# Kernel tuning notes

Measured on AMD Instinct MI355X. Metric: run time of the kernel, lower is better.

The kernel has to match this reference:

```python
import jax, jax.numpy as jnp
import numpy as np

N, E, D, H = 40000, 640000, 128, 8
DH = D // H  # out_feats per head
EPS = 1e-5


def _layernorm(x, g, b):
    mu = jnp.mean(x, axis=-1, keepdims=True)
    var = jnp.mean(jnp.square(x - mu), axis=-1, keepdims=True)
    return (x - mu) * jax.lax.rsqrt(var + EPS) * g + b


def setup_inputs() -> dict:
    key = jax.random.key(0)
    ks = jax.random.split(key, 12)
    s = 0.02
    return {
        "feat": jax.random.normal(ks[0], (N, D), dtype=jnp.float32),
        "src": jax.random.randint(ks[1], (E,), 0, N, dtype=jnp.int32),
        "dst": jax.random.randint(ks[2], (E,), 0, N, dtype=jnp.int32),
        "Wq": jax.random.normal(ks[3], (D, D), dtype=jnp.float32) * s,
        "Wk": jax.random.normal(ks[4], (D, D), dtype=jnp.float32) * s,
        "Wv": jax.random.normal(ks[5], (D, D), dtype=jnp.float32) * s,
        "ln1_g": jnp.ones((D,), jnp.float32),
        "ln1_b": jnp.zeros((D,), jnp.float32),
        "ln2_g": jnp.ones((D,), jnp.float32),
        "ln2_b": jnp.zeros((D,), jnp.float32),
        "W1": jax.random.normal(ks[6], (D, 4 * D), dtype=jnp.float32) * s,
        "b1": jnp.zeros((4 * D,), jnp.float32),
        "prelu_w": jnp.full((4 * D,), 0.25, jnp.float32),
        "W2": jax.random.normal(ks[7], (4 * D, D), dtype=jnp.float32) * s,
        "b2": jnp.zeros((D,), jnp.float32),
    }


def reference(feat, src, dst, Wq, Wk, Wv, ln1_g, ln1_b, ln2_g, ln2_b,
              W1, b1, prelu_w, W2, b2):
    n = feat.shape[0]
    feat_c = jax.lax.stop_gradient(feat)  # .clone().detach()
    q = (feat @ Wq).reshape(n, H, DH)
    k = (feat_c @ Wk).reshape(n, H, DH)
    v = (feat_c @ Wv).reshape(n, H, DH)

    # u_dot_v: per-edge, per-head dot product of k at src and q at dst
    scores = jnp.einsum('ehd,ehd->eh', k[src], q[dst]) / np.float32(np.sqrt(DH * H))

    # edge_softmax: softmax over incoming edges of each destination node
    smax = jax.ops.segment_max(scores, dst, num_segments=n)  # [N,H]
    sexp = jnp.exp(scores - smax[dst])
    ssum = jax.ops.segment_sum(sexp, dst, num_segments=n)
    a = sexp / ssum[dst]  # [E,H]  (attn_drop is eval no-op)

    # u_mul_e + sum: weighted scatter-aggregate of v[src] into dst
    msgs = v[src] * a[:, :, None]  # [E,H,DH]
    ft2 = jax.ops.segment_sum(msgs, dst, num_segments=n).reshape(n, D)

    rst = _layernorm(ft2 + feat, ln1_g, ln1_b)
    h = rst @ W1 + b1
    h = jnp.where(h >= 0, h, prelu_w * h)  # PReLU, per-channel
    ffn = h @ W2 + b2  # ffn_drop is eval no-op
    return _layernorm(rst + ffn, ln2_g, ln2_b)
```

## Files before the change

### kernel.cpp

```cpp
#include <hip/hip_runtime.h>
#include <hip/hip_bf16.h>
#include <math.h>

#define DIM 128
#define NHEAD 8
#define DHEAD 16
#define HID 512
#define LN_EPS 1e-5f
#define QSCALE 0.12751879104863297f

typedef __bf16 bf16x8 __attribute__((ext_vector_type(8)));
typedef float f32x4 __attribute__((ext_vector_type(4)));
typedef float f32x2 __attribute__((ext_vector_type(2)));
typedef _Float16 f16x2 __attribute__((ext_vector_type(2)));

__device__ inline float bf2f(unsigned int bits16) {
    return __uint_as_float(bits16 << 16);
}
__device__ inline unsigned short f2bf(float f) {
    unsigned int u = __float_as_uint(f);
    unsigned int r = u + 0x7fff + ((u >> 16) & 1);
    return (unsigned short)(r >> 16);
}
__device__ inline unsigned short f2h(float f) {
    _Float16 h = (_Float16)f;
    return __builtin_bit_cast(unsigned short, h);
}
__device__ inline unsigned short pk_fp8(float a, float b) {
    int r = __builtin_amdgcn_cvt_pk_fp8_f32(a, b, 0, false);
    return (unsigned short)(r & 0xffff);
}
template <bool HI>
__device__ inline f32x2 unpk_fp8(unsigned int w) {
    return __builtin_amdgcn_cvt_pk_f32_fp8((int)w, HI);
}
__device__ inline float fexp2(float x) { return __builtin_amdgcn_exp2f(x); }

__device__ inline void gload_lds16(const void* g, void* l) {
    __builtin_amdgcn_global_load_lds(
        (const __attribute__((address_space(1))) unsigned int*)g,
        (__attribute__((address_space(3))) unsigned int*)l, 16, 0, 0);
}

__global__ __launch_bounds__(256) void prep_kernel(
        int* counts, int Nn,
        const float* __restrict__ feat, unsigned short* __restrict__ featb,
        const float* __restrict__ Wq, const float* __restrict__ Wk, const float* __restrict__ Wv,
        unsigned short* __restrict__ Wqkvt,
        const float* __restrict__ W1, unsigned short* __restrict__ W1t,
        const float* __restrict__ W2, unsigned short* __restrict__ W2t,
        int zb, int fb) {
    int blk = blockIdx.x, t = threadIdx.x;
    if (blk < zb) {
        int i = blk * 1024 + t * 4;
        if (i < Nn) *(int4*)(counts + i) = make_int4(0, 0, 0, 0);
    } else if (blk < fb) {
        int i = (blk - zb) * 256 + t;
        if (i < Nn * 32) {
            float4 v = *(const float4*)(feat + (size_t)i * 4);
            ushort4 o;
            o.x = f2bf(v.x); o.y = f2bf(v.y); o.z = f2bf(v.z); o.w = f2bf(v.w);
            *(ushort4*)(featb + (size_t)i * 4) = o;
        }
    } else {
        int b2_ = blk - fb;
        if (b2_ < 192) {
            int sec = b2_ >> 6;
            const float* W = sec == 0 ? Wq : (sec == 1 ? Wk : Wv);
            int o = (b2_ & 63) * 256 + t;
            int oc = o >> 7, orow = o & 127;
            Wqkvt[sec * 16384 + o] = f2bf(W[(size_t)orow * 128 + oc]);
        } else if (b2_ < 448) {
            int o = (b2_ - 192) * 256 + t;
            int oc = o >> 7, orow = o & 127;
            W1t[o] = f2bf(W1[(size_t)orow * 512 + oc]);
        } else {
            int o = (b2_ - 448) * 256 + t;
            int oc = o >> 9, orow = o & 511;
            W2t[o] = f2bf(W2[(size_t)orow * 128 + oc]);
        }
    }
}


__global__ void count_kernel(const int* __restrict__ dst, int* counts, int E) {
    int e = blockIdx.x * blockDim.x + threadIdx.x;
    if (e < E) atomicAdd(&counts[dst[e]], 1);
}

__global__ __launch_bounds__(256) void scanA_kernel(const int* __restrict__ counts, int* bsum, int Nn) {
    int blk = blockIdx.x, t = threadIdx.x;
    int i = blk * 1024 + t * 4;
    int s = 0;
    if (i < Nn) { int4 x = *(const int4*)(counts + i); s = x.x + x.y + x.z + x.w; }
#pragma unroll
    for (int off = 1; off < 64; off <<= 1) s += __shfl_xor(s, off, 64);
    __shared__ int wt[4];
    if ((t & 63) == 0) wt[t >> 6] = s;
    __syncthreads();
    if (t == 0) bsum[blk] = wt[0] + wt[1] + wt[2] + wt[3];
}

__global__ __launch_bounds__(256) void scanC_kernel(int* counts, const int* __restrict__ bsum,
                                                    int* offsets, int Nn, int NCH) {
    int blk = blockIdx.x, t = threadIdx.x, lane = t & 63, wv = t >> 6;
    __shared__ int wt[4];
    __shared__ int base_s;
    if (wv == 0) {
        int v = (lane < NCH) ? bsum[lane] : 0;
        int s = v;
#pragma unroll
        for (int off = 1; off < 64; off <<= 1) {
            int u = __shfl_up(s, off, 64);
            if (lane >= off) s += u;
        }
        int basev = (blk > 0) ? __shfl(s, blk - 1, 64) : 0;
        int tot = __shfl(s, NCH - 1, 64);
        if (lane == 0) {
            base_s = basev;
            if (blk == 0) offsets[Nn] = tot;
        }
    }
    int i = blk * 1024 + t * 4;
    int4 x = make_int4(0, 0, 0, 0);
    if (i < Nn) x = *(const int4*)(counts + i);
    int ts = x.x + x.y + x.z + x.w;
    int s = ts;
#pragma unroll
    for (int off = 1; off < 64; off <<= 1) {
        int u = __shfl_up(s, off, 64);
        if (lane >= off) s += u;
    }
    if (lane == 63) wt[wv] = s;
    __syncthreads();
    int woff = 0;
    for (int wi = 0; wi < wv; ++wi) woff += wt[wi];
    int excl = base_s + woff + (s - ts);
    if (i < Nn) {
        int o0 = excl, o1 = o0 + x.x, o2 = o1 + x.y, o3 = o2 + x.z;
        *(int4*)(offsets + i) = make_int4(o0, o1, o2, o3);
        *(int4*)(counts + i) = make_int4(o0, o1, o2, o3);
    }
}

__global__ void fill_kernel(const int* __restrict__ dst, const int* __restrict__ src,
                            int* cursor, int* srcs, int E) {
    int e = blockIdx.x * blockDim.x + threadIdx.x;
    if (e < E) {
        int pos = atomicAdd(&cursor[dst[e]], 1);
        srcs[pos] = src[e];
    }
}

#define QST 136
__global__ __launch_bounds__(256) void qkv_gemm(
        const unsigned short* __restrict__ A, const unsigned short* __restrict__ Bt,
        unsigned short* __restrict__ qb, unsigned short* __restrict__ kvp) {
    __shared__ unsigned short smem[128 * QST];
    unsigned short* As = smem;
    unsigned short* Bs = smem + 4096;
    int t = threadIdx.x;
    int wave = t >> 6, lane = t & 63;
    int wr = wave >> 1, wc = wave & 1;
    int lrow = lane & 15, kq = lane >> 4;
    int m0 = blockIdx.y * 128;
    int region = blockIdx.x;
    int n0 = region * 128;
    int srow = t >> 2, scol8 = (t & 3) * 8;

    f32x4 acc[4][4] = {};
    for (int k0 = 0; k0 < 128; k0 += 32) {
        gload_lds16(A + (size_t)(m0 + srow) * 128 + k0 + scol8,      As + t * 8);
        gload_lds16(A + (size_t)(m0 + 64 + srow) * 128 + k0 + scol8, As + 2048 + t * 8);
        gload_lds16(Bt + (size_t)(n0 + srow) * 128 + k0 + scol8,      Bs + t * 8);
        gload_lds16(Bt + (size_t)(n0 + 64 + srow) * 128 + k0 + scol8, Bs + 2048 + t * 8);
        __syncthreads();
        bf16x8 af[4], bfr[4];
#pragma unroll
        for (int mi = 0; mi < 4; ++mi)
            af[mi] = *(const bf16x8*)(&As[(wr * 64 + mi * 16 + lrow) * 32 + kq * 8]);
#pragma unroll
        for (int ni = 0; ni < 4; ++ni)
            bfr[ni] = *(const bf16x8*)(&Bs[(wc * 64 + ni * 16 + lrow) * 32 + kq * 8]);
#pragma unroll
        for (int mi = 0; mi < 4; ++mi)
#pragma unroll
            for (int ni = 0; ni < 4; ++ni)
                acc[mi][ni] = __builtin_amdgcn_mfma_f32_16x16x32_bf16(af[mi], bfr[ni], acc[mi][ni], 0, 0, 0);
        __syncthreads();
    }

    float scale = (region == 0) ? QSCALE : 1.f;
#pragma unroll
    for (int ni = 0; ni < 4; ++ni) {
        int col = wc * 64 + ni * 16 + lrow;
#pragma unroll
        for (int mi = 0; mi < 4; ++mi) {
#pragma unroll
            for (int r = 0; r < 4; ++r) {
                int row = wr * 64 + mi * 16 + kq * 4 + r;
                smem[row * QST + col] = f2h(acc[mi][ni][r] * scale);
            }
        }
    }
    __syncthreads();
    if (region == 0) {
        unsigned short* outp = qb + (size_t)m0 * 128;
#pragma unroll
        for (int i = 0; i < 8; ++i) {
            int chunk = i * 256 + t;
            int row = chunk >> 4, c16 = chunk & 15;
            *(float4*)(outp + (size_t)chunk * 8) = *(const float4*)(smem + row * QST + c16 * 8);
        }
    } else {
        int off = region - 1;
        int row = t >> 1, half = t & 1;
        unsigned short* dstp = kvp + (size_t)(m0 + row) * 128 + off;
        const unsigned short* sp = smem + row * QST;
#pragma unroll
        for (int jj = 0; jj < 32; ++jj) {
            int j = half * 32 + jj;
            float f0 = (float)__builtin_bit_cast(_Float16, sp[2 * j]);
            float f1 = (float)__builtin_bit_cast(_Float16, sp[2 * j + 1]);
            dstp[2 * j] = pk_fp8(f0, f1);
        }
    }
}

__global__ __launch_bounds__(256) void agg_ln1_kernel(
        const unsigned short* __restrict__ qb, const unsigned short* __restrict__ kvp,
        const float* __restrict__ feat,
        const int* __restrict__ srcs, const int* __restrict__ offsets,
        const float* __restrict__ g, const float* __restrict__ b,
        unsigned short* __restrict__ rstb, int n) {
    int node = blockIdx.x * 4 + (threadIdx.x >> 6);
    int lane = threadIdx.x & 63;
    if (node >= n) return;

    unsigned int qw = ((const unsigned int*)qb)[(size_t)node * 64 + lane];
    f16x2 qp = __builtin_bit_cast(f16x2, qw);
    float q0 = (float)qp.x, q1 = (float)qp.y;
    const unsigned int* kv32 = (const unsigned int*)kvp;

    int beg = offsets[node], end = offsets[node + 1];
    float l = 0.f, a0 = 0.f, a1 = 0.f;

    int idx = beg;
    for (; idx + 8 <= end; idx += 8) {
        int s[8];
#pragma unroll
        for (int i = 0; i < 8; ++i) s[i] = srcs[idx + i];
        unsigned int w[8];
#pragma unroll
        for (int i = 0; i < 8; ++i) w[i] = kv32[(size_t)s[i] * 64 + lane];
        float sc[8];
#pragma unroll
        for (int i = 0; i < 8; ++i) {
            f32x2 kk = unpk_fp8<false>(w[i]);
            float p = fmaf(kk.x, q0, kk.y * q1);
            p += __shfl_xor(p, 1, 8);
            p += __shfl_xor(p, 2, 8);
            p += __shfl_xor(p, 4, 8);
            sc[i] = fminf(fmaxf(p, -30.f), 30.f);
        }
#pragma unroll
        for (int i = 0; i < 8; ++i) {
            float ww = fexp2(sc[i]);
            f32x2 vv = unpk_fp8<true>(w[i]);
            l += ww;
            a0 = fmaf(vv.x, ww, a0);
            a1 = fmaf(vv.y, ww, a1);
        }
    }
    for (; idx < end; ++idx) {
        int s = srcs[idx];
        unsigned int w = kv32[(size_t)s * 64 + lane];
        f32x2 kk = unpk_fp8<false>(w);
        float p = fmaf(kk.x, q0, kk.y * q1);
        p += __shfl_xor(p, 1, 8);
        p += __shfl_xor(p, 2, 8);
        p += __shfl_xor(p, 4, 8);
        float ww = fexp2(fminf(fmaxf(p, -30.f), 30.f));
        f32x2 vv = unpk_fp8<true>(w);
        l += ww;
        a0 = fmaf(vv.x, ww, a0);
        a1 = fmaf(vv.y, ww, a1);
    }

    float inv = (l > 0.f) ? 1.f / l : 0.f;
    float2 fv = *(const float2*)(feat + (size_t)node * DIM + 2 * lane);
    float x0 = a0 * inv + fv.x;
    float x1 = a1 * inv + fv.y;

    float s1 = x0 + x1;
    float s2 = x0 * x0 + x1 * x1;
#pragma unroll
    for (int off = 1; off < 64; off <<= 1) {
        s1 += __shfl_xor(s1, off, 64);
        s2 += __shfl_xor(s2, off, 64);
    }
    float mean = s1 * (1.f / DIM);
    float var = s2 * (1.f / DIM) - mean * mean;
    float rinv = rsqrtf(var + LN_EPS);
    float g0 = g[2 * lane], g1 = g[2 * lane + 1];
    float b0 = b[2 * lane], b1 = b[2 * lane + 1];
    float o0 = (x0 - mean) * rinv * g0 + b0;
    float o1 = (x1 - mean) * rinv * g1 + b1;
    unsigned int packed = (unsigned int)f2bf(o0) | ((unsigned int)f2bf(o1) << 16);
    ((unsigned int*)rstb)[(size_t)node * 64 + lane] = packed;
}

__global__ __launch_bounds__(256) void ffn1_gemm(
        const unsigned short* __restrict__ A, const unsigned short* __restrict__ Bt,
        unsigned short* __restrict__ hid,
        const float* __restrict__ b1, const float* __restrict__ prelu) {
    __shared__ unsigned short smem[128 * QST];
    unsigned short* As = smem;
    unsigned short* Bs = smem + 4096;
    int t = threadIdx.x;
    int wave = t >> 6, lane = t & 63;
    int wr = wave >> 1, wc = wave & 1;
    int lrow = lane & 15, kq = lane >> 4;
    int m0 = blockIdx.y * 128;
    int n0 = blockIdx.x * 128;
    int srow = t >> 2, scol8 = (t & 3) * 8;

    f32x4 acc[4][4] = {};
    for (int k0 = 0; k0 < 128; k0 += 32) {
        gload_lds16(A + (size_t)(m0 + srow) * 128 + k0 + scol8,      As + t * 8);
        gload_lds16(A + (size_t)(m0 + 64 + srow) * 128 + k0 + scol8, As + 2048 + t * 8);
        gload_lds16(Bt + (size_t)(n0 + srow) * 128 + k0 + scol8,      Bs + t * 8);
        gload_lds16(Bt + (size_t)(n0 + 64 + srow) * 128 + k0 + scol8, Bs + 2048 + t * 8);
        __syncthreads();
        bf16x8 af[4], bfr[4];
#pragma unroll
        for (int mi = 0; mi < 4; ++mi)
            af[mi] = *(const bf16x8*)(&As[(wr * 64 + mi * 16 + lrow) * 32 + kq * 8]);
#pragma unroll
        for (int ni = 0; ni < 4; ++ni)
            bfr[ni] = *(const bf16x8*)(&Bs[(wc * 64 + ni * 16 + lrow) * 32 + kq * 8]);
#pragma unroll
        for (int mi = 0; mi < 4; ++mi)
#pragma unroll
            for (int ni = 0; ni < 4; ++ni)
                acc[mi][ni] = __builtin_amdgcn_mfma_f32_16x16x32_bf16(af[mi], bfr[ni], acc[mi][ni], 0, 0, 0);
        __syncthreads();
    }

#pragma unroll
    for (int ni = 0; ni < 4; ++ni) {
        int col = wc * 64 + ni * 16 + lrow;
        int cg = n0 + col;
        float biv = b1[cg], pwv = prelu[cg];
#pragma unroll
        for (int mi = 0; mi < 4; ++mi) {
#pragma unroll
            for (int r = 0; r < 4; ++r) {
                int row = wr * 64 + mi * 16 + kq * 4 + r;
                float v = acc[mi][ni][r] + biv;
                v = v >= 0.f ? v : pwv * v;
                smem[row * QST + col] = f2bf(v);
            }
        }
    }
    __syncthreads();
#pragma unroll
    for (int i = 0; i < 8; ++i) {
        int chunk = i * 256 + t;
        int row = chunk >> 4, c16 = chunk & 15;
        *(float4*)(hid + (size_t)(m0 + row) * 512 + n0 + c16 * 8) =
            *(const float4*)(smem + row * QST + c16 * 8);
    }
}

__global__ __launch_bounds__(256) void ffn2_ln2_kernel(
        const unsigned short* __restrict__ hid, const unsigned short* __restrict__ W2t,
        const unsigned short* __restrict__ rstb,
        const float* __restrict__ b2, const float* __restrict__ g, const float* __restrict__ bb,
        float* __restrict__ out, int Nn) {
    __shared__ unsigned short As[64 * 32];
    __shared__ unsigned short Bs[128 * 32];
    __shared__ float redS[64][4];
    __shared__ float redQ[64][4];
    int t = threadIdx.x;
    int wave = t >> 6, lane = t & 63;
    int lrow = lane & 15, kq = lane >> 4;
    int m0 = blockIdx.x * 64;
    int srow = t >> 2, scol8 = (t & 3) * 8;

    f32x4 acc[4][2] = {};
    for (int k0 = 0; k0 < 512; k0 += 32) {
        gload_lds16(hid + (size_t)(m0 + srow) * 512 + k0 + scol8, As + t * 8);
        gload_lds16(W2t + (size_t)srow * 512 + k0 + scol8,        Bs + t * 8);
        gload_lds16(W2t + (size_t)(64 + srow) * 512 + k0 + scol8, Bs + 2048 + t * 8);
        __syncthreads();
        bf16x8 af[4], bfr[2];
#pragma unroll
        for (int mi = 0; mi < 4; ++mi)
            af[mi] = *(const bf16x8*)(&As[(mi * 16 + lrow) * 32 + kq * 8]);
#pragma unroll
        for (int ni = 0; ni < 2; ++ni)
            bfr[ni] = *(const bf16x8*)(&Bs[(wave * 32 + ni * 16 + lrow) * 32 + kq * 8]);
#pragma unroll
        for (int mi = 0; mi < 4; ++mi)
#pragma unroll
            for (int ni = 0; ni < 2; ++ni)
                acc[mi][ni] = __builtin_amdgcn_mfma_f32_16x16x32_bf16(af[mi], bfr[ni], acc[mi][ni], 0, 0, 0);
        __syncthreads();
    }

    float b2v[2], gv[2], bv[2];
    int cols[2];
#pragma unroll
    for (int ni = 0; ni < 2; ++ni) {
        cols[ni] = wave * 32 + ni * 16 + lrow;
        b2v[ni] = b2[cols[ni]]; gv[ni] = g[cols[ni]]; bv[ni] = bb[cols[ni]];
    }
#pragma unroll
    for (int mi = 0; mi < 4; ++mi) {
#pragma unroll
        for (int r = 0; r < 4; ++r) {
            int rloc = mi * 16 + kq * 4 + r;
            int row = m0 + rloc;
            float ps = 0.f, pq = 0.f;
#pragma unroll
            for (int ni = 0; ni < 2; ++ni) {
                float rsv = bf2f(rstb[(size_t)row * 128 + cols[ni]]);
                float v = acc[mi][ni][r] + b2v[ni] + rsv;
                acc[mi][ni][r] = v;
                ps += v; pq += v * v;
            }
#pragma unroll
            for (int off = 1; off < 16; off <<= 1) {
                ps += __shfl_xor(ps, off, 16);
                pq += __shfl_xor(pq, off, 16);
            }
            if (lrow == 0) { redS[rloc][wave] = ps; redQ[rloc][wave] = pq; }
        }
    }
    __syncthreads();
#pragma unroll
    for (int mi = 0; mi < 4; ++mi) {
#pragma unroll
        for (int r = 0; r < 4; ++r) {
            int rloc = mi * 16 + kq * 4 + r;
            int row = m0 + rloc;
            float s1 = redS[rloc][0] + redS[rloc][1] + redS[rloc][2] + redS[rloc][3];
            float sq = redQ[rloc][0] + redQ[rloc][1] + redQ[rloc][2] + redQ[rloc][3];
            float mean = s1 * (1.f / DIM);
            float var = sq * (1.f / DIM) - mean * mean;
            float rs = rsqrtf(var + LN_EPS);
            if (row < Nn) {
#pragma unroll
                for (int ni = 0; ni < 2; ++ni)
                    out[(size_t)row * 128 + cols[ni]] =
                        (acc[mi][ni][r] - mean) * rs * gv[ni] + bv[ni];
            }
        }
    }
}


extern "C" void kernel_launch(void* const* d_in, const int* in_sizes, int n_in,
                              void* d_out, int out_size, void* d_ws, size_t ws_size,
                              hipStream_t stream) {
    const float* feat   = (const float*)d_in[0];
    const int*   src    = (const int*)d_in[1];
    const int*   dst    = (const int*)d_in[2];
    const float* Wq     = (const float*)d_in[3];
    const float* Wk     = (const float*)d_in[4];
    const float* Wv     = (const float*)d_in[5];
    const float* ln1_g  = (const float*)d_in[6];
    const float* ln1_b  = (const float*)d_in[7];
    const float* ln2_g  = (const float*)d_in[8];
    const float* ln2_b  = (const float*)d_in[9];
    const float* W1     = (const float*)d_in[10];
    const float* b1     = (const float*)d_in[11];
    const float* prelu  = (const float*)d_in[12];
    const float* W2     = (const float*)d_in[13];
    const float* b2     = (const float*)d_in[14];
    float* out = (float*)d_out;

    const int Nn = in_sizes[0] / DIM;
    const int E  = in_sizes[1];
    const int MP = (Nn + 127) & ~127;

    char* w = (char*)d_ws;
    unsigned short* qb   = (unsigned short*)w; w += (size_t)MP * DIM * 2;
    unsigned short* kvp  = (unsigned short*)w; w += (size_t)MP * DIM * 2;
    unsigned short* rstb = (unsigned short*)w; w += (size_t)MP * DIM * 2;
    unsigned short* featb= (unsigned short*)w; w += (size_t)MP * DIM * 2;
    unsigned short* hid  = (unsigned short*)w; w += (size_t)MP * HID * 2;
    unsigned short* Wqkvt= (unsigned short*)w; w += 3 * DIM * DIM * 2;
    unsigned short* W1t  = (unsigned short*)w; w += (size_t)HID * DIM * 2;
    unsigned short* W2t  = (unsigned short*)w; w += (size_t)DIM * HID * 2;
    int* counts  = (int*)w;  w += (size_t)Nn * 4;
    int* offsets = (int*)w;  w += (size_t)(Nn + 4) * 4;
    int* bsum    = (int*)w;  w += 64 * 4;
    int* srcs    = (int*)w;

    const int NCH = (Nn + 1023) / 1024;
    const int zb = NCH;
    const int fb = zb + Nn / 8;

    prep_kernel<<<fb + 192 + 256 + 256, 256, 0, stream>>>(
        counts, Nn, feat, featb, Wq, Wk, Wv, Wqkvt, W1, W1t, W2, W2t, zb, fb);

    count_kernel<<<(E + 255) / 256, 256, 0, stream>>>(dst, counts, E);
    scanA_kernel<<<NCH, 256, 0, stream>>>(counts, bsum, Nn);
    scanC_kernel<<<NCH, 256, 0, stream>>>(counts, bsum, offsets, Nn, NCH);
    fill_kernel<<<(E + 255) / 256, 256, 0, stream>>>(dst, src, counts, srcs, E);

    {
        dim3 grid(3, MP / 128);
        qkv_gemm<<<grid, 256, 0, stream>>>(featb, Wqkvt, qb, kvp);
    }

    agg_ln1_kernel<<<(Nn + 3) / 4, 256, 0, stream>>>(qb, kvp, feat, srcs, offsets,
                                                     ln1_g, ln1_b, rstb, Nn);

    {
        dim3 grid(4, MP / 128);
        ffn1_gemm<<<grid, 256, 0, stream>>>(rstb, W1t, hid, b1, prelu);
    }

    ffn2_ln2_kernel<<<MP / 64, 256, 0, stream>>>(hid, W2t, rstb, b2, ln2_g, ln2_b, out, Nn);
}
```

Before: 279.2 us.

## Fuse edge count into prep, fuse CSR fill with QKV GEMM, split K/V fp8 layout

Folds the per-edge count atomics into the prep kernel and the CSR fill into the QKV GEMM launch as extra blocks, which removes two kernel launches and lets the independent work overlap. Counter zeroing now uses hipMemsetAsync. K and V are stored as separate 128-byte fp8 halves per node and written with wide vectorized stores instead of strided 2-byte stores. The aggregation loop is unified with masked tail handling, at the cost of two gathers per edge and some wasted lanes on short neighbor lists.

```diff
diff --git a/kernel.cpp b/kernel.cpp
--- a/kernel.cpp
+++ b/kernel.cpp
@@ -26,13 +26,15 @@
     _Float16 h = (_Float16)f;
     return __builtin_bit_cast(unsigned short, h);
 }
+__device__ inline float h2f(unsigned short h) {
+    return (float)__builtin_bit_cast(_Float16, h);
+}
 __device__ inline unsigned short pk_fp8(float a, float b) {
     int r = __builtin_amdgcn_cvt_pk_fp8_f32(a, b, 0, false);
     return (unsigned short)(r & 0xffff);
 }
-template <bool HI>
-__device__ inline f32x2 unpk_fp8(unsigned int w) {
-    return __builtin_amdgcn_cvt_pk_f32_fp8((int)w, HI);
+__device__ inline f32x2 unpk_fp8_lo(unsigned int w) {
+    return __builtin_amdgcn_cvt_pk_f32_fp8((int)w, false);
 }
 __device__ inline float fexp2(float x) { return __builtin_amdgcn_exp2f(x); }
 
@@ -42,27 +44,24 @@
         (__attribute__((address_space(3))) unsigned int*)l, 16, 0, 0);
 }
 
-__global__ __launch_bounds__(256) void prep_kernel(
+__global__ __launch_bounds__(256) void prep_count_kernel(
         int* counts, int Nn,
         const float* __restrict__ feat, unsigned short* __restrict__ featb,
         const float* __restrict__ Wq, const float* __restrict__ Wk, const float* __restrict__ Wv,
         unsigned short* __restrict__ Wqkvt,
         const float* __restrict__ W1, unsigned short* __restrict__ W1t,
         const float* __restrict__ W2, unsigned short* __restrict__ W2t,
-        int zb, int fb) {
+        const int* __restrict__ dst, int E, int fb, int wb) {
     int blk = blockIdx.x, t = threadIdx.x;
-    if (blk < zb) {
-        int i = blk * 1024 + t * 4;
-        if (i < Nn) *(int4*)(counts + i) = make_int4(0, 0, 0, 0);
-    } else if (blk < fb) {
-        int i = (blk - zb) * 256 + t;
+    if (blk < fb) {
+        int i = blk * 256 + t;
         if (i < Nn * 32) {
             float4 v = *(const float4*)(feat + (size_t)i * 4);
             ushort4 o;
             o.x = f2bf(v.x); o.y = f2bf(v.y); o.z = f2bf(v.z); o.w = f2bf(v.w);
             *(ushort4*)(featb + (size_t)i * 4) = o;
         }
-    } else {
+    } else if (blk < wb) {
         int b2_ = blk - fb;
         if (b2_ < 192) {
             int sec = b2_ >> 6;
@@ -79,14 +78,20 @@
             int oc = o >> 9, orow = o & 511;
             W2t[o] = f2bf(W2[(size_t)orow * 128 + oc]);
         }
-    }
-}
-
-
-__global__ void count_kernel(const int* __restrict__ dst, int* counts, int E) {
-    int e = blockIdx.x * blockDim.x + threadIdx.x;
-    if (e < E) atomicAdd(&counts[dst[e]], 1);
-}
+    } else {
+        int e0 = (blk - wb) * 1024 + t * 4;
+        if (e0 + 3 < E) {
+            int4 d = *(const int4*)(dst + e0);
+            atomicAdd(&counts[d.x], 1);
+            atomicAdd(&counts[d.y], 1);
+            atomicAdd(&counts[d.z], 1);
+            atomicAdd(&counts[d.w], 1);
+        } else {
+            for (int e = e0; e < E; ++e) atomicAdd(&counts[dst[e]], 1);
+        }
+    }
+}
+
 
 __global__ __launch_bounds__(256) void scanA_kernel(const int* __restrict__ counts, int* bsum, int Nn) {
     int blk = blockIdx.x, t = threadIdx.x;
@@ -143,28 +148,36 @@
     }
 }
 
-__global__ void fill_kernel(const int* __restrict__ dst, const int* __restrict__ src,
-                            int* cursor, int* srcs, int E) {
-    int e = blockIdx.x * blockDim.x + threadIdx.x;
-    if (e < E) {
-        int pos = atomicAdd(&cursor[dst[e]], 1);
-        srcs[pos] = src[e];
-    }
-}
-
 #define QST 136
-__global__ __launch_bounds__(256) void qkv_gemm(
+__global__ __launch_bounds__(256) void fill_qkv_kernel(
+        const int* __restrict__ dst, const int* __restrict__ src,
+        int* cursor, int* srcs, int E, int cb,
         const unsigned short* __restrict__ A, const unsigned short* __restrict__ Bt,
-        unsigned short* __restrict__ qb, unsigned short* __restrict__ kvp) {
+        unsigned short* __restrict__ qb, unsigned char* __restrict__ kv8) {
+    int blk = blockIdx.x, t = threadIdx.x;
+    if (blk < cb) {
+        int e0 = blk * 1024 + t * 4;
+        if (e0 + 3 < E) {
+            int4 d = *(const int4*)(dst + e0);
+            int4 sv = *(const int4*)(src + e0);
+            srcs[atomicAdd(&cursor[d.x], 1)] = sv.x;
+            srcs[atomicAdd(&cursor[d.y], 1)] = sv.y;
+            srcs[atomicAdd(&cursor[d.z], 1)] = sv.z;
+            srcs[atomicAdd(&cursor[d.w], 1)] = sv.w;
+        } else {
+            for (int e = e0; e < E; ++e) srcs[atomicAdd(&cursor[dst[e]], 1)] = src[e];
+        }
+        return;
+    }
     __shared__ unsigned short smem[128 * QST];
     unsigned short* As = smem;
     unsigned short* Bs = smem + 4096;
-    int t = threadIdx.x;
+    int q = blk - cb;
+    int region = q % 3;
+    int m0 = (q / 3) * 128;
     int wave = t >> 6, lane = t & 63;
     int wr = wave >> 1, wc = wave & 1;
     int lrow = lane & 15, kq = lane >> 4;
-    int m0 = blockIdx.y * 128;
-    int region = blockIdx.x;
     int n0 = region * 128;
     int srow = t >> 2, scol8 = (t & 3) * 8;
 
@@ -213,22 +226,27 @@
             *(float4*)(outp + (size_t)chunk * 8) = *(const float4*)(smem + row * QST + c16 * 8);
         }
     } else {
-        int off = region - 1;
-        int row = t >> 1, half = t & 1;
-        unsigned short* dstp = kvp + (size_t)(m0 + row) * 128 + off;
-        const unsigned short* sp = smem + row * QST;
-#pragma unroll
-        for (int jj = 0; jj < 32; ++jj) {
-            int j = half * 32 + jj;
-            float f0 = (float)__builtin_bit_cast(_Float16, sp[2 * j]);
-            float f1 = (float)__builtin_bit_cast(_Float16, sp[2 * j + 1]);
-            dstp[2 * j] = pk_fp8(f0, f1);
+        int half = region - 1;
+#pragma unroll
+        for (int i = 0; i < 4; ++i) {
+            int chunk = i * 256 + t;
+            int row = chunk >> 3, seg = chunk & 7;
+            const unsigned short* sp = smem + row * QST + seg * 16;
+            unsigned int ow[4];
+#pragma unroll
+            for (int j = 0; j < 4; ++j) {
+                unsigned int lo = pk_fp8(h2f(sp[4 * j]), h2f(sp[4 * j + 1]));
+                unsigned int hi = pk_fp8(h2f(sp[4 * j + 2]), h2f(sp[4 * j + 3]));
+                ow[j] = lo | (hi << 16);
+            }
+            *(uint4*)(kv8 + (size_t)(m0 + row) * 256 + half * 128 + seg * 16) =
+                make_uint4(ow[0], ow[1], ow[2], ow[3]);
         }
     }
 }
 
 __global__ __launch_bounds__(256) void agg_ln1_kernel(
-        const unsigned short* __restrict__ qb, const unsigned short* __restrict__ kvp,
+        const unsigned short* __restrict__ qb, const unsigned short* __restrict__ kvu,
         const float* __restrict__ feat,
         const int* __restrict__ srcs, const int* __restrict__ offsets,
         const float* __restrict__ g, const float* __restrict__ b,
@@ -240,51 +258,47 @@
     unsigned int qw = ((const unsigned int*)qb)[(size_t)node * 64 + lane];
     f16x2 qp = __builtin_bit_cast(f16x2, qw);
     float q0 = (float)qp.x, q1 = (float)qp.y;
-    const unsigned int* kv32 = (const unsigned int*)kvp;
 
     int beg = offsets[node], end = offsets[node + 1];
     float l = 0.f, a0 = 0.f, a1 = 0.f;
 
-    int idx = beg;
-    for (; idx + 8 <= end; idx += 8) {
-        int s[8];
-#pragma unroll
-        for (int i = 0; i < 8; ++i) s[i] = srcs[idx + i];
-        unsigned int w[8];
-#pragma unroll
-        for (int i = 0; i < 8; ++i) w[i] = kv32[(size_t)s[i] * 64 + lane];
+    for (int idx = beg; idx < end; idx += 8) {
+        int sa[8];
+#pragma unroll
+        for (int i = 0; i < 8; ++i) {
+            int ii = idx + i;
+            sa[i] = (ii < end) ? srcs[ii] : -1;
+        }
+        unsigned int kw[8], vw[8];
+#pragma unroll
+        for (int i = 0; i < 8; ++i) {
+            int s = sa[i] < 0 ? 0 : sa[i];
+            kw[i] = kvu[(size_t)s * 128 + lane];
+        }
+#pragma unroll
+        for (int i = 0; i < 8; ++i) {
+            int s = sa[i] < 0 ? 0 : sa[i];
+            vw[i] = kvu[(size_t)s * 128 + 64 + lane];
+        }
         float sc[8];
 #pragma unroll
         for (int i = 0; i < 8; ++i) {
-            f32x2 kk = unpk_fp8<false>(w[i]);
+            f32x2 kk = unpk_fp8_lo(kw[i]);
             float p = fmaf(kk.x, q0, kk.y * q1);
             p += __shfl_xor(p, 1, 8);
             p += __shfl_xor(p, 2, 8);
             p += __shfl_xor(p, 4, 8);
-            sc[i] = fminf(fmaxf(p, -30.f), 30.f);
+            p = fminf(fmaxf(p, -30.f), 30.f);
+            sc[i] = (sa[i] < 0) ? -1000.f : p;
         }
 #pragma unroll
         for (int i = 0; i < 8; ++i) {
             float ww = fexp2(sc[i]);
-            f32x2 vv = unpk_fp8<true>(w[i]);
+            f32x2 vv = unpk_fp8_lo(vw[i]);
             l += ww;
             a0 = fmaf(vv.x, ww, a0);
             a1 = fmaf(vv.y, ww, a1);
         }
-    }
-    for (; idx < end; ++idx) {
-        int s = srcs[idx];
-        unsigned int w = kv32[(size_t)s * 64 + lane];
-        f32x2 kk = unpk_fp8<false>(w);
-        float p = fmaf(kk.x, q0, kk.y * q1);
-        p += __shfl_xor(p, 1, 8);
-        p += __shfl_xor(p, 2, 8);
-        p += __shfl_xor(p, 4, 8);
-        float ww = fexp2(fminf(fmaxf(p, -30.f), 30.f));
-        f32x2 vv = unpk_fp8<true>(w);
-        l += ww;
-        a0 = fmaf(vv.x, ww, a0);
-        a1 = fmaf(vv.y, ww, a1);
     }
 
     float inv = (l > 0.f) ? 1.f / l : 0.f;
@@ -487,7 +501,7 @@
 
     char* w = (char*)d_ws;
     unsigned short* qb   = (unsigned short*)w; w += (size_t)MP * DIM * 2;
-    unsigned short* kvp  = (unsigned short*)w; w += (size_t)MP * DIM * 2;
+    unsigned char*  kv8  = (unsigned char*)w;  w += (size_t)MP * 256;
     unsigned short* rstb = (unsigned short*)w; w += (size_t)MP * DIM * 2;
     unsigned short* featb= (unsigned short*)w; w += (size_t)MP * DIM * 2;
     unsigned short* hid  = (unsigned short*)w; w += (size_t)MP * HID * 2;
@@ -500,24 +514,23 @@
     int* srcs    = (int*)w;
 
     const int NCH = (Nn + 1023) / 1024;
-    const int zb = NCH;
-    const int fb = zb + Nn / 8;
-
-    prep_kernel<<<fb + 192 + 256 + 256, 256, 0, stream>>>(
-        counts, Nn, feat, featb, Wq, Wk, Wv, Wqkvt, W1, W1t, W2, W2t, zb, fb);
-
-    count_kernel<<<(E + 255) / 256, 256, 0, stream>>>(dst, counts, E);
+    const int FB  = Nn / 8;
+    const int WB  = FB + 704;
+    const int CB  = (E + 1023) / 1024;
+
+    hipMemsetAsync(counts, 0, (size_t)Nn * 4, stream);
+
+    prep_count_kernel<<<WB + CB, 256, 0, stream>>>(
+        counts, Nn, feat, featb, Wq, Wk, Wv, Wqkvt, W1, W1t, W2, W2t, dst, E, FB, WB);
+
     scanA_kernel<<<NCH, 256, 0, stream>>>(counts, bsum, Nn);
     scanC_kernel<<<NCH, 256, 0, stream>>>(counts, bsum, offsets, Nn, NCH);
-    fill_kernel<<<(E + 255) / 256, 256, 0, stream>>>(dst, src, counts, srcs, E);
-
-    {
-        dim3 grid(3, MP / 128);
-        qkv_gemm<<<grid, 256, 0, stream>>>(featb, Wqkvt, qb, kvp);
-    }
-
-    agg_ln1_kernel<<<(Nn + 3) / 4, 256, 0, stream>>>(qb, kvp, feat, srcs, offsets,
-                                                     ln1_g, ln1_b, rstb, Nn);
+
+    fill_qkv_kernel<<<CB + 3 * (MP / 128), 256, 0, stream>>>(
+        dst, src, counts, srcs, E, CB, featb, Wqkvt, qb, kv8);
+
+    agg_ln1_kernel<<<(Nn + 3) / 4, 256, 0, stream>>>(qb, (const unsigned short*)kv8, feat,
+                                                     srcs, offsets, ln1_g, ln1_b, rstb, Nn);
 
     {
         dim3 grid(4, MP / 128);
```

Result: faster. 258.7 us (-7.4%).
